# Kernel optimization log

Hardware: AMD Instinct MI355X
Metric: run time of the kernel (lower is better)

Reference implementation:

```python
import jax, jax.numpy as jnp
import numpy as np

N_EL, N_NB, DIM = 8192, 24, 256
CUTOFF = 5.0
F0, F1 = 32, 16
N_ENV = 8
N_FEAT = 4  # [dist, dx, dy, dz]


def setup_inputs() -> dict:
    key = jax.random.key(0)
    ks = jax.random.split(key, 24)
    d = {}
    d['elec'] = jax.random.normal(ks[0], (N_EL, DIM), jnp.float32)
    d['msg'] = jax.random.normal(ks[1], (N_EL, DIM), jnp.float32)
    # positions inside a box of half the cutoff so pairs are within range
    d['r'] = jax.random.uniform(ks[2], (N_EL, 3), jnp.float32) * (0.5 * CUTOFF)
    d['r_nb'] = jax.random.uniform(ks[3], (N_EL, N_NB, 3), jnp.float32) * (0.5 * CUTOFF)
    d['s'] = jax.random.randint(ks[4], (N_EL,), 0, 2, jnp.int32)
    d['s_nb'] = jax.random.randint(ks[5], (N_EL, N_NB), 0, 2, jnp.int32)
    d['hinit_nb'] = jax.random.normal(ks[6], (N_EL, N_NB, DIM), jnp.float32)
    # parameters
    def lecun(k, shape):
        fan_in = shape[0]
        return jax.random.normal(k, shape, jnp.float32) / np.float32(np.sqrt(fan_in))
    d['W_in'] = lecun(ks[7], (DIM, DIM)); d['b_in'] = jnp.zeros((DIM,), jnp.float32)
    d['ee_scales'] = jax.random.uniform(ks[8], (N_ENV,), jnp.float32, 0.5, CUTOFF)
    d['ee_kernel'] = lecun(ks[9], (N_FEAT, F0))
    d['ee_bias'] = 2.0 * jax.random.normal(ks[10], (F0,), jnp.float32)
    d['Wf'] = lecun(ks[11], (F0 + N_ENV, F1)); d['bf'] = jnp.zeros((F1,), jnp.float32)
    d['Wsame'] = lecun(ks[12], (F1, DIM))
    d['Wdiff'] = lecun(ks[13], (F1, DIM))
    d['W1'] = lecun(ks[14], (DIM, DIM)); d['b1'] = jnp.zeros((DIM,), jnp.float32)
    d['W2'] = lecun(ks[15], (DIM, DIM)); d['b2'] = jnp.zeros((DIM,), jnp.float32)
    d['W3'] = lecun(ks[16], (DIM, DIM)); d['b3'] = jnp.zeros((DIM,), jnp.float32)
    d['scale'] = jnp.float32(1.0)  # FixedScalingFactor (identity at init)
    return d


def _forward(elec, msg, r, r_nb, s, s_nb, hinit_nb,
             W_in, b_in, ee_scales, ee_kernel, ee_bias, Wf, bf,
             Wsame, Wdiff, W1, b1, W2, b2, W3, b3, scale):
    silu = jax.nn.silu
    elec1 = silu(elec @ W_in + b_in)                       # [N, D]
    # get_diff_features: [dist, dx, dy, dz]
    diff = r_nb - r[:, None, :]                             # [N, K, 3]
    dist = jnp.sqrt(jnp.sum(diff * diff, -1) + 1e-12)       # [N, K]
    feats = jnp.concatenate([dist[..., None], diff], -1)    # [N, K, 4]
    spin_mask = s[:, None] == s_nb                          # [N, K]
    # PairwiseFilter: MLP on diff-features + radial envelopes, smooth cutoff
    env = jnp.exp(-jnp.square(dist[..., None] / ee_scales)) # [N, K, E]
    h = silu(feats @ ee_kernel + ee_bias)                   # [N, K, F0]
    h = jnp.concatenate([h, env], -1)                       # [N, K, F0+E]
    x = dist / CUTOFF
    cut = jnp.where(dist < CUTOFF, jnp.square(1.0 - x) * (1.0 + 2.0 * x), 0.0)
    beta = (h @ Wf + bf) * cut[..., None]                   # [N, K, F1]
    gamma = jnp.where(spin_mask[..., None], beta @ Wsame, beta @ Wdiff)  # [N, K, D]
    hinit_msg = jnp.einsum('nid,nid->nd', silu(elec1[:, None] + hinit_nb), gamma)
    out = silu(elec1 @ W1 + b1 + hinit_msg)
    out = silu(out @ W2 + b2 + msg)
    out = silu(out @ W3 + b3)
    return (out + elec1) * scale


def reference(elec, msg, r, r_nb, s, s_nb, hinit_nb,
              W_in, b_in, ee_scales, ee_kernel, ee_bias, Wf, bf,
              Wsame, Wdiff, W1, b1, W2, b2, W3, b3, scale):
    return _forward(elec, msg, r, r_nb, s, s_nb, hinit_nb,
                    W_in, b_in, ee_scales, ee_kernel, ee_bias, Wf, bf,
                    Wsame, Wdiff, W1, b1, W2, b2, W3, b3, scale)
```

## Files before the change

kernel.cpp:

```cpp
#include <hip/hip_runtime.h>

#define DIM 256
#define PDIM 260
#define PD2  264
#define SBPITCH 20
#define NNB 24
#define NEL 8192
#define ROWS 16
#define NT 512
#define CUTOFF 5.0f

typedef unsigned int u32;
typedef unsigned short u16;
typedef __attribute__((ext_vector_type(8))) short bf16x8;
typedef __attribute__((ext_vector_type(4))) float f32x4;

#define GL_LDS(g, l) __builtin_amdgcn_global_load_lds( \
    (const __attribute__((address_space(1))) void*)(g), \
    (__attribute__((address_space(3))) void*)(l), 16, 0, 0)

__device__ __forceinline__ u16 f2b(float f){
  union{float f;u32 i;}v; v.f=f;
  u32 r = v.i + 0x7fffu + ((v.i>>16)&1u);
  return (u16)(r>>16);
}
__device__ __forceinline__ float b2f(u16 u){
  union{u32 i;float f;}v; v.i = ((u32)u)<<16; return v.f;
}
__device__ __forceinline__ float fast_silu(float x){
  float e = __builtin_amdgcn_exp2f(-1.44269504088896340f * x);
  return x * __builtin_amdgcn_rcpf(1.0f + e);
}

__global__ __launch_bounds__(256)
void wprep(const float* __restrict__ W0, const float* __restrict__ W1,
           const float* __restrict__ W2, const float* __restrict__ W3,
           const float* __restrict__ Wsame, const float* __restrict__ Wdiff,
           u16* __restrict__ ws){
  if (blockIdx.x < 1024){
    const int mat = blockIdx.x >> 8;
    const int n   = blockIdx.x & 255;
    const int k   = threadIdx.x;
    const float* W = (mat==0)?W0:(mat==1)?W1:(mat==2)?W2:W3;
    ws[(mat<<16) + (n<<8) + k] = f2b(W[(k<<8) + n]);
  } else {
    const int n = threadIdx.x;
    u16* dst = ws + 4*65536 + n*32;
    #pragma unroll
    for (int kk = 0; kk < 16; kk++){
      dst[kk]    = f2b(Wsame[kk*DIM + n]);
      dst[16+kk] = f2b(Wdiff[kk*DIM + n]);
    }
  }
}

template<int MODE, int ABF16>
__device__ __forceinline__ void gemm_mfma(
    const void* A, u16* sE1b, float* sR1,
    const u16* __restrict__ Wt, const float* __restrict__ bias,
    const float* __restrict__ extraGbl, float* __restrict__ outGbl,
    float scl, int n0, int t)
{
  const int lane = t & 63;
  const int ln   = lane & 15;
  const int quad = lane >> 4;
  const int nt0  = (t >> 6) << 1;
  f32x4 acc0 = {0.f,0.f,0.f,0.f};
  f32x4 acc1 = {0.f,0.f,0.f,0.f};
  const u16* bp0 = Wt + (nt0*16 + ln)*DIM;
  const u16* bp1 = bp0 + 16*DIM;
  #pragma unroll
  for (int ks = 0; ks < 8; ks++){
    const int k0 = ks*32 + quad*8;
    bf16x8 af;
    if (ABF16){
      af = *(const bf16x8*)((const u16*)A + ln*PD2 + k0);
    } else {
      const float* arow = (const float*)A + ln*PDIM;
      float4 a01 = *(const float4*)(arow + k0);
      float4 a23 = *(const float4*)(arow + k0 + 4);
      af[0]=(short)f2b(a01.x); af[1]=(short)f2b(a01.y);
      af[2]=(short)f2b(a01.z); af[3]=(short)f2b(a01.w);
      af[4]=(short)f2b(a23.x); af[5]=(short)f2b(a23.y);
      af[6]=(short)f2b(a23.z); af[7]=(short)f2b(a23.w);
    }
    bf16x8 b0 = *(const bf16x8*)(bp0 + k0);
    bf16x8 b1 = *(const bf16x8*)(bp1 + k0);
    acc0 = __builtin_amdgcn_mfma_f32_16x16x32_bf16(af, b0, acc0, 0, 0, 0);
    acc1 = __builtin_amdgcn_mfma_f32_16x16x32_bf16(af, b1, acc1, 0, 0, 0);
  }
  if (MODE == 2) __syncthreads();
  #pragma unroll
  for (int r = 0; r < 4; r++){
    const int m = quad*4 + r;
    #pragma unroll
    for (int tt = 0; tt < 2; tt++){
      const int n = (nt0+tt)*16 + ln;
      float v = (tt ? acc1[r] : acc0[r]) + bias[n];
      if (MODE == 1) v += sR1[m*PDIM + n];
      if (MODE == 2) v += extraGbl[(size_t)(n0+m)*DIM + n];
      v = fast_silu(v);
      if (MODE == 0)      sE1b[m*PD2 + n] = f2b(v);
      else if (MODE == 3) outGbl[(size_t)(n0+m)*DIM + n] = (v + b2f(sE1b[m*PD2 + n])) * scl;
      else                sR1[m*PDIM + n] = v;
    }
  }
}

__global__ __launch_bounds__(NT, 4)
void fused_moon_kernel(
    const float* __restrict__ elec, const float* __restrict__ msg,
    const float* __restrict__ rpos, const float* __restrict__ rnb,
    const int* __restrict__ s,    const int* __restrict__ snb,
    const float* __restrict__ hinit,
    const float* __restrict__ bin,
    const float* __restrict__ eesc, const float* __restrict__ eek,
    const float* __restrict__ eeb,  const float* __restrict__ Wf,
    const float* __restrict__ bfb,
    const float* __restrict__ b1, const float* __restrict__ b2,
    const float* __restrict__ b3,
    const float* __restrict__ scalep,
    const u16* __restrict__ Wt,
    float* __restrict__ out)
{
  __shared__ float sR1[ROWS*PDIM];
  __shared__ u16   sE1b[ROWS*PD2];
  __shared__ u16   sBC[NNB*16*SBPITCH];
  __shared__ u32   sMaskB[ROWS];
  __shared__ float sH[8][2][512];
  const int t  = threadIdx.x;
  const int n0 = blockIdx.x * ROWS;
  const int lane = t & 63;
  const int w    = t >> 6;
  const int C0   = w << 5;

  const float* hsrc = hinit
      + (size_t)(n0 + (lane & 15)) * NNB * DIM + C0 + ((lane >> 4) << 2);
  float* sHw0 = &sH[w][0][0];
  float* sHw1 = &sH[w][1][0];
  GL_LDS(hsrc + 0*DIM,      sHw0);
  GL_LDS(hsrc + 0*DIM + 16, sHw0 + 256);
  GL_LDS(hsrc + 1*DIM,      sHw1);
  GL_LDS(hsrc + 1*DIM + 16, sHw1 + 256);

  if (t < ROWS) sMaskB[t] = 0u;
  {
    const float4* ep = (const float4*)elec;
    #pragma unroll
    for (int h = 0; h < 2; h++){
      const int idx = t + h*NT;
      float4 v = ep[(size_t)n0*64 + idx];
      *(float4*)&sR1[(idx>>6)*PDIM + (idx&63)*4] = v;
    }
  }
  __syncthreads();

  gemm_mfma<0,0>(sR1, sE1b, sR1, Wt, bin, nullptr, nullptr, 0.f, n0, t);

  if (t < ROWS*NNB) {
    const int rr = t / NNB;
    const int k  = t - rr*NNB;
    const int n  = n0 + rr;
    const float* rp  = rpos + n*3;
    const float* rnp = rnb + (n*NNB + k)*3;
    float dx = rnp[0] - rp[0];
    float dy = rnp[1] - rp[1];
    float dz = rnp[2] - rp[2];
    float dist = sqrtf(dx*dx + dy*dy + dz*dz + 1e-12f);
    float feats[4] = {dist, dx, dy, dz};
    float h[32];
    #pragma unroll
    for (int f4 = 0; f4 < 8; f4++){
      float4 a4 = *(const float4*)&eeb[4*f4];
      float av[4] = {a4.x, a4.y, a4.z, a4.w};
      #pragma unroll
      for (int i = 0; i < 4; i++){
        float4 kv = *(const float4*)&eek[i*32 + 4*f4];
        av[0]+=feats[i]*kv.x; av[1]+=feats[i]*kv.y; av[2]+=feats[i]*kv.z; av[3]+=feats[i]*kv.w;
      }
      h[4*f4+0]=fast_silu(av[0]); h[4*f4+1]=fast_silu(av[1]);
      h[4*f4+2]=fast_silu(av[2]); h[4*f4+3]=fast_silu(av[3]);
    }
    float env[8];
    #pragma unroll
    for (int e = 0; e < 8; e++){
      float q = dist * __builtin_amdgcn_rcpf(eesc[e]);
      env[e] = __builtin_amdgcn_exp2f(-1.44269504088896340f * q * q);
    }
    float xx = dist * (1.0f/CUTOFF);
    float cut = (dist < CUTOFF) ? (1.0f-xx)*(1.0f-xx)*(1.0f+2.0f*xx) : 0.0f;
    u16* rowp = &sBC[(k*16 + rr)*SBPITCH];
    #pragma unroll
    for (int j4 = 0; j4 < 4; j4++){
      float4 a4 = *(const float4*)&bfb[4*j4];
      float av[4] = {a4.x, a4.y, a4.z, a4.w};
      #pragma unroll
      for (int f = 0; f < 40; f++){
        float val = (f < 32) ? h[f] : env[f-32];
        float4 wv = *(const float4*)&Wf[f*16 + 4*j4];
        av[0]+=val*wv.x; av[1]+=val*wv.y; av[2]+=val*wv.z; av[3]+=val*wv.w;
      }
      ushort4 bv;
      bv.x = f2b(av[0]*cut); bv.y = f2b(av[1]*cut);
      bv.z = f2b(av[2]*cut); bv.w = f2b(av[3]*cut);
      *(ushort4*)(rowp + 4*j4) = bv;
    }
    if (s[n] == snb[n*NNB + k]) atomicOr(&sMaskB[rr], 1u << k);
  }
  __syncthreads();

  {
    const int ln   = lane & 15;
    const int quad = lane >> 4;
    const int nA   = C0 + (quad << 2);
    const u16* Wcat = Wt + 4*65536;
    bf16x8 bs0 = *(const bf16x8*)(Wcat + (C0 + ln)*32 + quad*8);
    bf16x8 bs1 = *(const bf16x8*)(Wcat + (C0 + 16 + ln)*32 + quad*8);

    float e1A[4], e1B[4];
    {
      ushort4 ea = *(const ushort4*)&sE1b[ln*PD2 + nA];
      ushort4 eb = *(const ushort4*)&sE1b[ln*PD2 + nA + 16];
      e1A[0]=b2f(ea.x); e1A[1]=b2f(ea.y); e1A[2]=b2f(ea.z); e1A[3]=b2f(ea.w);
      e1B[0]=b2f(eb.x); e1B[1]=b2f(eb.y); e1B[2]=b2f(eb.z); e1B[3]=b2f(eb.w);
    }
    const u32 mb = sMaskB[ln];
    float hmA[4] = {0.f,0.f,0.f,0.f};
    float hmB[4] = {0.f,0.f,0.f,0.f};
    for (int k = 0; k < NNB; k++){
      if (k < NNB-1) { asm volatile("s_waitcnt vmcnt(2)" ::: "memory"); }
      else           { asm volatile("s_waitcnt vmcnt(0)" ::: "memory"); }
      float* sHw = (k & 1) ? sHw1 : sHw0;
      float4 hv0 = *(const float4*)&sHw[lane*4];
      float4 hv1 = *(const float4*)&sHw[256 + lane*4];
      bf16x8 b8 = *(const bf16x8*)(&sBC[(k*16 + ln)*SBPITCH + (quad&1)*8]);
      const u16 km = (u16)((((u32)(quad>>1) ^ ((mb>>k)&1u)) != 0u) ? 0xFFFFu : 0u);
      bf16x8 af;
      #pragma unroll
      for (int j = 0; j < 8; j++) af[j] = (short)((u16)b8[j] & km);
      __builtin_amdgcn_sched_barrier(0);
      if (k + 2 < NNB){
        GL_LDS(hsrc + (size_t)(k+2)*DIM,      sHw);
        GL_LDS(hsrc + (size_t)(k+2)*DIM + 16, sHw + 256);
      }
      f32x4 z = {0.f,0.f,0.f,0.f};
      f32x4 g0 = __builtin_amdgcn_mfma_f32_16x16x32_bf16(bs0, af, z, 0, 0, 0);
      f32x4 g1 = __builtin_amdgcn_mfma_f32_16x16x32_bf16(bs1, af, z, 0, 0, 0);
      hmA[0] += fast_silu(e1A[0]+hv0.x)*g0[0];
      hmA[1] += fast_silu(e1A[1]+hv0.y)*g0[1];
      hmA[2] += fast_silu(e1A[2]+hv0.z)*g0[2];
      hmA[3] += fast_silu(e1A[3]+hv0.w)*g0[3];
      hmB[0] += fast_silu(e1B[0]+hv1.x)*g1[0];
      hmB[1] += fast_silu(e1B[1]+hv1.y)*g1[1];
      hmB[2] += fast_silu(e1B[2]+hv1.z)*g1[2];
      hmB[3] += fast_silu(e1B[3]+hv1.w)*g1[3];
    }
    *(float4*)&sR1[ln*PDIM + nA]      = make_float4(hmA[0],hmA[1],hmA[2],hmA[3]);
    *(float4*)&sR1[ln*PDIM + nA + 16] = make_float4(hmB[0],hmB[1],hmB[2],hmB[3]);
  }
  __syncthreads();

  const float scl = scalep[0];

  gemm_mfma<1,1>(sE1b, sE1b, sR1, Wt + (1<<16), b1, nullptr, nullptr, 0.f, n0, t);
  __syncthreads();
  gemm_mfma<2,0>(sR1, sE1b, sR1, Wt + (2<<16), b2, msg, nullptr, 0.f, n0, t);
  __syncthreads();
  gemm_mfma<3,0>(sR1, sE1b, sR1, Wt + (3<<16), b3, nullptr, out, scl, n0, t);
}

extern "C" void kernel_launch(void* const* d_in, const int* in_sizes, int n_in,
                              void* d_out, int out_size, void* d_ws, size_t ws_size,
                              hipStream_t stream) {
  (void)in_sizes; (void)n_in; (void)ws_size; (void)out_size;
  const float* elec  = (const float*)d_in[0];
  const float* msg   = (const float*)d_in[1];
  const float* rpos  = (const float*)d_in[2];
  const float* rnb   = (const float*)d_in[3];
  const int*   s     = (const int*)d_in[4];
  const int*   snb   = (const int*)d_in[5];
  const float* hinit = (const float*)d_in[6];
  const float* Win   = (const float*)d_in[7];
  const float* bin   = (const float*)d_in[8];
  const float* eesc  = (const float*)d_in[9];
  const float* eek   = (const float*)d_in[10];
  const float* eeb   = (const float*)d_in[11];
  const float* Wf    = (const float*)d_in[12];
  const float* bfb   = (const float*)d_in[13];
  const float* Wsame = (const float*)d_in[14];
  const float* Wdiff = (const float*)d_in[15];
  const float* W1    = (const float*)d_in[16];
  const float* b1    = (const float*)d_in[17];
  const float* W2    = (const float*)d_in[18];
  const float* b2    = (const float*)d_in[19];
  const float* W3    = (const float*)d_in[20];
  const float* b3    = (const float*)d_in[21];
  const float* scl   = (const float*)d_in[22];
  float* outp        = (float*)d_out;
  u16*   wt          = (u16*)d_ws;

  wprep<<<dim3(1025), dim3(256), 0, stream>>>(Win, W1, W2, W3, Wsame, Wdiff, wt);
  fused_moon_kernel<<<dim3(NEL/ROWS), dim3(NT), 0, stream>>>(
      elec, msg, rpos, rnb, s, snb, hinit,
      bin, eesc, eek, eeb, Wf, bfb,
      b1, b2, b3, scl, wt, outp);
}
```

Before: 369.8 us.

## Split fused kernel into GEMM, message, and trailing-GEMM kernels

```diff
diff --git a/kernel.cpp b/kernel.cpp
--- a/kernel.cpp
+++ b/kernel.cpp
@@ -9,6 +9,7 @@
 #define ROWS 16
 #define NT 512
 #define CUTOFF 5.0f
+#define E1_OFF 524288
 
 typedef unsigned int u32;
 typedef unsigned short u16;
@@ -97,37 +98,70 @@
     for (int tt = 0; tt < 2; tt++){
       const int n = (nt0+tt)*16 + ln;
       float v = (tt ? acc1[r] : acc0[r]) + bias[n];
-      if (MODE == 1) v += sR1[m*PDIM + n];
       if (MODE == 2) v += extraGbl[(size_t)(n0+m)*DIM + n];
       v = fast_silu(v);
-      if (MODE == 0)      sE1b[m*PD2 + n] = f2b(v);
-      else if (MODE == 3) outGbl[(size_t)(n0+m)*DIM + n] = (v + b2f(sE1b[m*PD2 + n])) * scl;
-      else                sR1[m*PDIM + n] = v;
+      if (MODE == 3) outGbl[(size_t)(n0+m)*DIM + n] = (v + b2f(sE1b[m*PD2 + n])) * scl;
+      else           sR1[m*PDIM + n] = v;
+    }
+  }
+}
+
+__global__ __launch_bounds__(NT, 8)
+void k1_gemm1(const float* __restrict__ elec, const float* __restrict__ bin,
+              const u16* __restrict__ Wt, u16* __restrict__ elec1g)
+{
+  const int t  = threadIdx.x;
+  const int n0 = blockIdx.x * ROWS;
+  const int lane = t & 63;
+  const int ln   = lane & 15;
+  const int quad = lane >> 4;
+  const int nt0  = (t >> 6) << 1;
+  f32x4 acc0 = {0.f,0.f,0.f,0.f};
+  f32x4 acc1 = {0.f,0.f,0.f,0.f};
+  const u16* bp0 = Wt + (nt0*16 + ln)*DIM;
+  const u16* bp1 = bp0 + 16*DIM;
+  const float* arow = elec + (size_t)(n0 + ln)*DIM;
+  #pragma unroll
+  for (int ks = 0; ks < 8; ks++){
+    const int k0 = ks*32 + quad*8;
+    float4 a01 = *(const float4*)(arow + k0);
+    float4 a23 = *(const float4*)(arow + k0 + 4);
+    bf16x8 af;
+    af[0]=(short)f2b(a01.x); af[1]=(short)f2b(a01.y);
+    af[2]=(short)f2b(a01.z); af[3]=(short)f2b(a01.w);
+    af[4]=(short)f2b(a23.x); af[5]=(short)f2b(a23.y);
+    af[6]=(short)f2b(a23.z); af[7]=(short)f2b(a23.w);
+    bf16x8 b0 = *(const bf16x8*)(bp0 + k0);
+    bf16x8 b1 = *(const bf16x8*)(bp1 + k0);
+    acc0 = __builtin_amdgcn_mfma_f32_16x16x32_bf16(af, b0, acc0, 0, 0, 0);
+    acc1 = __builtin_amdgcn_mfma_f32_16x16x32_bf16(af, b1, acc1, 0, 0, 0);
+  }
+  #pragma unroll
+  for (int r = 0; r < 4; r++){
+    const int m = quad*4 + r;
+    #pragma unroll
+    for (int tt = 0; tt < 2; tt++){
+      const int n = (nt0+tt)*16 + ln;
+      float v = fast_silu((tt ? acc1[r] : acc0[r]) + bin[n]);
+      elec1g[(size_t)(n0+m)*DIM + n] = f2b(v);
     }
   }
 }
 
 __global__ __launch_bounds__(NT, 4)
-void fused_moon_kernel(
-    const float* __restrict__ elec, const float* __restrict__ msg,
-    const float* __restrict__ rpos, const float* __restrict__ rnb,
-    const int* __restrict__ s,    const int* __restrict__ snb,
-    const float* __restrict__ hinit,
-    const float* __restrict__ bin,
-    const float* __restrict__ eesc, const float* __restrict__ eek,
-    const float* __restrict__ eeb,  const float* __restrict__ Wf,
-    const float* __restrict__ bfb,
-    const float* __restrict__ b1, const float* __restrict__ b2,
-    const float* __restrict__ b3,
-    const float* __restrict__ scalep,
-    const u16* __restrict__ Wt,
-    float* __restrict__ out)
+void k2_msg(const float* __restrict__ rpos, const float* __restrict__ rnb,
+            const int* __restrict__ s, const int* __restrict__ snb,
+            const float* __restrict__ hinit,
+            const float* __restrict__ eesc, const float* __restrict__ eek,
+            const float* __restrict__ eeb,  const float* __restrict__ Wf,
+            const float* __restrict__ bfb,
+            const u16* __restrict__ Wt, const u16* __restrict__ elec1g,
+            float* __restrict__ hmsg)
 {
-  __shared__ float sR1[ROWS*PDIM];
-  __shared__ u16   sE1b[ROWS*PD2];
   __shared__ u16   sBC[NNB*16*SBPITCH];
   __shared__ u32   sMaskB[ROWS];
   __shared__ float sH[8][2][512];
+  __shared__ float sPar[824];
   const int t  = threadIdx.x;
   const int n0 = blockIdx.x * ROWS;
   const int lane = t & 63;
@@ -144,18 +178,16 @@
   GL_LDS(hsrc + 1*DIM + 16, sHw1 + 256);
 
   if (t < ROWS) sMaskB[t] = 0u;
-  {
-    const float4* ep = (const float4*)elec;
-    #pragma unroll
-    for (int h = 0; h < 2; h++){
-      const int idx = t + h*NT;
-      float4 v = ep[(size_t)n0*64 + idx];
-      *(float4*)&sR1[(idx>>6)*PDIM + (idx&63)*4] = v;
-    }
-  }
-  __syncthreads();
-
-  gemm_mfma<0,0>(sR1, sE1b, sR1, Wt, bin, nullptr, nullptr, 0.f, n0, t);
+  for (int i = t; i < 824; i += NT){
+    float v;
+    if (i < 640)      v = Wf[i];
+    else if (i < 768) v = eek[i-640];
+    else if (i < 800) v = eeb[i-768];
+    else if (i < 816) v = bfb[i-800];
+    else              v = eesc[i-816];
+    sPar[i] = v;
+  }
+  __syncthreads();
 
   if (t < ROWS*NNB) {
     const int rr = t / NNB;
@@ -171,11 +203,11 @@
     float h[32];
     #pragma unroll
     for (int f4 = 0; f4 < 8; f4++){
-      float4 a4 = *(const float4*)&eeb[4*f4];
+      float4 a4 = *(const float4*)&sPar[768 + 4*f4];
       float av[4] = {a4.x, a4.y, a4.z, a4.w};
       #pragma unroll
       for (int i = 0; i < 4; i++){
-        float4 kv = *(const float4*)&eek[i*32 + 4*f4];
+        float4 kv = *(const float4*)&sPar[640 + i*32 + 4*f4];
         av[0]+=feats[i]*kv.x; av[1]+=feats[i]*kv.y; av[2]+=feats[i]*kv.z; av[3]+=feats[i]*kv.w;
       }
       h[4*f4+0]=fast_silu(av[0]); h[4*f4+1]=fast_silu(av[1]);
@@ -184,7 +216,7 @@
     float env[8];
     #pragma unroll
     for (int e = 0; e < 8; e++){
-      float q = dist * __builtin_amdgcn_rcpf(eesc[e]);
+      float q = dist * __builtin_amdgcn_rcpf(sPar[816 + e]);
       env[e] = __builtin_amdgcn_exp2f(-1.44269504088896340f * q * q);
     }
     float xx = dist * (1.0f/CUTOFF);
@@ -192,12 +224,12 @@
     u16* rowp = &sBC[(k*16 + rr)*SBPITCH];
     #pragma unroll
     for (int j4 = 0; j4 < 4; j4++){
-      float4 a4 = *(const float4*)&bfb[4*j4];
+      float4 a4 = *(const float4*)&sPar[800 + 4*j4];
       float av[4] = {a4.x, a4.y, a4.z, a4.w};
       #pragma unroll
       for (int f = 0; f < 40; f++){
         float val = (f < 32) ? h[f] : env[f-32];
-        float4 wv = *(const float4*)&Wf[f*16 + 4*j4];
+        float4 wv = *(const float4*)&sPar[f*16 + 4*j4];
         av[0]+=val*wv.x; av[1]+=val*wv.y; av[2]+=val*wv.z; av[3]+=val*wv.w;
       }
       ushort4 bv;
@@ -219,8 +251,8 @@
 
     float e1A[4], e1B[4];
     {
-      ushort4 ea = *(const ushort4*)&sE1b[ln*PD2 + nA];
-      ushort4 eb = *(const ushort4*)&sE1b[ln*PD2 + nA + 16];
+      ushort4 ea = *(const ushort4*)&elec1g[(size_t)(n0+ln)*DIM + nA];
+      ushort4 eb = *(const ushort4*)&elec1g[(size_t)(n0+ln)*DIM + nA + 16];
       e1A[0]=b2f(ea.x); e1A[1]=b2f(ea.y); e1A[2]=b2f(ea.z); e1A[3]=b2f(ea.w);
       e1B[0]=b2f(eb.x); e1B[1]=b2f(eb.y); e1B[2]=b2f(eb.z); e1B[3]=b2f(eb.w);
     }
@@ -255,14 +287,36 @@
       hmB[2] += fast_silu(e1B[2]+hv1.z)*g1[2];
       hmB[3] += fast_silu(e1B[3]+hv1.w)*g1[3];
     }
-    *(float4*)&sR1[ln*PDIM + nA]      = make_float4(hmA[0],hmA[1],hmA[2],hmA[3]);
-    *(float4*)&sR1[ln*PDIM + nA + 16] = make_float4(hmB[0],hmB[1],hmB[2],hmB[3]);
+    *(float4*)&hmsg[(size_t)(n0+ln)*DIM + nA]      = make_float4(hmA[0],hmA[1],hmA[2],hmA[3]);
+    *(float4*)&hmsg[(size_t)(n0+ln)*DIM + nA + 16] = make_float4(hmB[0],hmB[1],hmB[2],hmB[3]);
+  }
+}
+
+__global__ __launch_bounds__(NT, 8)
+void k3_gemms(const float* __restrict__ msg, const u16* __restrict__ elec1g,
+              const float* __restrict__ b1, const float* __restrict__ b2,
+              const float* __restrict__ b3, const float* __restrict__ scalep,
+              const u16* __restrict__ Wt, float* __restrict__ out)
+{
+  __shared__ float sR1[ROWS*PDIM];
+  __shared__ u16   sE1b[ROWS*PD2];
+  const int t  = threadIdx.x;
+  const int n0 = blockIdx.x * ROWS;
+
+  {
+    const u32* e1u = (const u32*)elec1g;
+    #pragma unroll
+    for (int h = 0; h < 8; h++){
+      const int i   = t + h*NT;
+      const int row = i >> 7;
+      const int c2  = i & 127;
+      *(u32*)&sE1b[row*PD2 + 2*c2] = e1u[(size_t)(n0+row)*128 + c2];
+    }
   }
   __syncthreads();
 
   const float scl = scalep[0];
-
-  gemm_mfma<1,1>(sE1b, sE1b, sR1, Wt + (1<<16), b1, nullptr, nullptr, 0.f, n0, t);
+  gemm_mfma<2,1>(sE1b, sE1b, sR1, Wt + (1<<16), b1, out, nullptr, 0.f, n0, t);
   __syncthreads();
   gemm_mfma<2,0>(sR1, sE1b, sR1, Wt + (2<<16), b2, msg, nullptr, 0.f, n0, t);
   __syncthreads();
@@ -298,10 +352,12 @@
   const float* scl   = (const float*)d_in[22];
   float* outp        = (float*)d_out;
   u16*   wt          = (u16*)d_ws;
+  u16*   elec1g      = wt + E1_OFF;
 
   wprep<<<dim3(1025), dim3(256), 0, stream>>>(Win, W1, W2, W3, Wsame, Wdiff, wt);
-  fused_moon_kernel<<<dim3(NEL/ROWS), dim3(NT), 0, stream>>>(
-      elec, msg, rpos, rnb, s, snb, hinit,
-      bin, eesc, eek, eeb, Wf, bfb,
-      b1, b2, b3, scl, wt, outp);
-}
+  k1_gemm1<<<dim3(NEL/ROWS), dim3(NT), 0, stream>>>(elec, bin, wt, elec1g);
+  k2_msg<<<dim3(NEL/ROWS), dim3(NT), 0, stream>>>(
+      rpos, rnb, s, snb, hinit, eesc, eek, eeb, Wf, bfb, wt, elec1g, outp);
+  k3_gemms<<<dim3(NEL/ROWS), dim3(NT), 0, stream>>>(
+      msg, elec1g, b1, b2, b3, scl, wt, outp);
+}
```

After: 396.8 us. 7.3% more time.
